# Optimization experiments

Hardware: AMD Instinct MI355X
Metric: run time of the kernel (lower is better)

The kernel has to match this reference:

```python
import jax, jax.numpy as jnp
import numpy as np

NB, H, C, HID, EMB = 4, 12, 1024, 768, 512
E, M, L, SPAN = 22, 4, 16, 32
TD, INTER = 20, 256
NN = E + E * M + L
NREL, NLAYERS = 3, 4

def _build_adj():
    # static relational adjacency: r0 entity<->its mentions, r1 mention<->co-entity mention, r2 mention<->link
    A = np.zeros((NREL, NN, NN), np.float32)
    for e in range(E):
        for m in range(M):
            mi = E + e * M + m
            A[0, e, mi] = A[0, mi, e] = 1.0
            for m2 in range(M):
                if m2 != m:
                    A[1, mi, E + e * M + m2] = 1.0
            li = E + E * M + ((e * M + m) % L)
            A[2, mi, li] = A[2, li, mi] = 1.0
    A = A / (A.sum(-1, keepdims=True) + 1e-5)
    return jnp.asarray(A)

_ADJ = _build_adj()
_TYPES = np.concatenate([np.zeros(E, np.int32), np.ones(E * M, np.int32), np.full(L, 2, np.int32)])

def _forward(sequence_output, attention, W_trans, b_trans, type_embed,
             rgcn_Wrel0, rgcn_Wself0, rgcn_Wrel, rgcn_Wself,
             fs_w1, fs_b1, fs_g1, fs_be1, fs_w2, fs_b2, fs_g2, fs_be2,
             fc_w1, fc_b1, fc_g1, fc_be1, fc_w2, fc_b2, fc_g2, fc_be2,
             cr_w1, cr_b1, cr_w2, cr_b2, cr_w3, cr_b3,
             mention_idx, link_start):
    n = sequence_output.shape[0]
    b = jnp.arange(n)[:, None, None]
    seq = sequence_output @ W_trans + b_trans            # [n,C,EMB] extractor_trans
    attq = attention.transpose(0, 2, 1, 3)               # [n,C,H,C] query-major
    # --- make_graph: mention / entity nodes (gather + logsumexp pooling) ---
    m_rep = seq[b, mention_idx]                          # [n,E,M,EMB]
    m_att = attq[b, mention_idx]                         # [n,E,M,H,C]
    e_rep = jax.nn.logsumexp(m_rep, axis=2)              # [n,E,EMB]
    e_att = m_att.mean(axis=2)                           # [n,E,H,C]
    # --- link nodes: attention-weighted span pooling ---
    idx = link_start[:, :, None] + jnp.arange(SPAN)      # [n,L,SPAN]
    span = seq[b, idx]                                   # [n,L,SPAN,EMB]
    att_rows = attq[b, idx]                              # [n,L,SPAN,H,C]
    col_idx = jnp.broadcast_to(idx[:, :, None, None, :], (n, L, SPAN, H, SPAN))
    block = jnp.take_along_axis(att_rows, col_idx, axis=4).mean(axis=3)  # [n,L,SPAN,SPAN]
    link_rep = jnp.einsum('nlst,nltd->nld', block, span) / SPAN          # [n,L,EMB]
    # --- node matrix + type embedding ---
    nodes = jnp.concatenate([e_rep, m_rep.reshape(n, E * M, EMB), link_rep], axis=1)
    tfeat = jnp.broadcast_to(type_embed[_TYPES][None], (n, NN, TD))
    h = jnp.concatenate([nodes, tfeat], axis=-1)         # [n,NN,EMB+TD]
    # --- RGCN ---
    def rgcn_layer(hh, Wrel, Wself):
        msg = jnp.einsum('rij,njd,rdo->nio', _ADJ, hh, Wrel)
        return jax.nn.relu(msg + hh @ Wself)
    h = rgcn_layer(h, rgcn_Wrel0, rgcn_Wself0)
    for l in range(NLAYERS - 1):
        h = rgcn_layer(h, rgcn_Wrel[l], rgcn_Wself[l])
    # --- relation_map: structure + attention-weighted context ---
    entity_stru = h[:, :E]                               # [n,E,EMB]
    ea = e_att.mean(axis=2)                              # [n,E,C]
    ea = ea / (ea.sum(-1, keepdims=True) + 1e-5)
    e_ctx = jnp.einsum('nec,ncd->ned', ea, seq)          # [n,E,EMB]
    ec = entity_stru + e_ctx
    fmap = (ec[:, :, None, :] * ec[:, None, :, :]).transpose(0, 3, 1, 2)  # [n,EMB,E,E]
    # --- SE fusion (fusion_s / fusion_c, BN in eval form) ---
    conv1x1 = lambda x, w, bb: jnp.einsum('nchw,oc->nohw', x, w) + bb[None, :, None, None]
    bn = lambda x, g, be: x * g[None, :, None, None] + be[None, :, None, None]
    s = bn(conv1x1(jax.nn.relu(bn(conv1x1(fmap, fs_w1, fs_b1), fs_g1, fs_be1)), fs_w2, fs_b2), fs_g2, fs_be2)
    pooled = fmap.mean(axis=(2, 3), keepdims=True)
    cb = bn(conv1x1(jax.nn.relu(bn(conv1x1(pooled, fc_w1, fc_b1), fc_g1, fc_be1)), fc_w2, fc_b2), fc_g2, fc_be2)
    fused = fmap * jax.nn.sigmoid(s + cb)
    # --- conv_reason 5x5 blocks ---
    dn = ('NCHW', 'OIHW', 'NCHW')
    conv = lambda x, w, bb: jax.lax.conv_general_dilated(x, w, (1, 1), 'SAME', dimension_numbers=dn) + bb[None, :, None, None]
    r = jax.nn.relu(conv(fused, cr_w1, cr_b1))
    r = jax.nn.relu(conv(r, cr_w2, cr_b2))
    return jax.nn.relu(conv(r, cr_w3, cr_b3))            # [n,EMB,E,E]

def setup_inputs():
    key = jax.random.key(0)
    ks = jax.random.split(key, 24)
    p = lambda k, sh: jax.random.normal(k, sh, jnp.float32) * 0.02
    z = lambda sh: jnp.zeros(sh, jnp.float32)
    o = lambda sh: jnp.ones(sh, jnp.float32)
    return {
        'sequence_output': jax.random.normal(ks[0], (NB, C, HID), jnp.float32),
        'attention': jax.random.uniform(ks[1], (NB, H, C, C), jnp.float32),
        'W_trans': p(ks[2], (HID, EMB)), 'b_trans': z((EMB,)),
        'type_embed': p(ks[3], (3, TD)),
        'rgcn_Wrel0': p(ks[4], (NREL, EMB + TD, EMB)), 'rgcn_Wself0': p(ks[5], (EMB + TD, EMB)),
        'rgcn_Wrel': p(ks[6], (NLAYERS - 1, NREL, EMB, EMB)), 'rgcn_Wself': p(ks[7], (NLAYERS - 1, EMB, EMB)),
        'fs_w1': p(ks[8], (INTER, EMB)), 'fs_b1': z((INTER,)), 'fs_g1': o((INTER,)), 'fs_be1': z((INTER,)),
        'fs_w2': p(ks[9], (EMB, INTER)), 'fs_b2': z((EMB,)), 'fs_g2': o((EMB,)), 'fs_be2': z((EMB,)),
        'fc_w1': p(ks[10], (INTER, EMB)), 'fc_b1': z((INTER,)), 'fc_g1': o((INTER,)), 'fc_be1': z((INTER,)),
        'fc_w2': p(ks[11], (EMB, INTER)), 'fc_b2': z((EMB,)), 'fc_g2': o((EMB,)), 'fc_be2': z((EMB,)),
        'cr_w1': p(ks[12], (INTER, EMB, 5, 5)), 'cr_b1': z((INTER,)),
        'cr_w2': p(ks[13], (INTER, INTER, 5, 5)), 'cr_b2': z((INTER,)),
        'cr_w3': p(ks[14], (EMB, INTER, 5, 5)), 'cr_b3': z((EMB,)),
        'mention_idx': jax.random.randint(ks[15], (NB, E, M), 0, C),
        'link_start': jnp.sort(jax.random.randint(ks[16], (NB, L), 0, C - SPAN), axis=-1),
    }

def reference(sequence_output, attention, W_trans, b_trans, type_embed,
              rgcn_Wrel0, rgcn_Wself0, rgcn_Wrel, rgcn_Wself,
              fs_w1, fs_b1, fs_g1, fs_be1, fs_w2, fs_b2, fs_g2, fs_be2,
              fc_w1, fc_b1, fc_g1, fc_be1, fc_w2, fc_b2, fc_g2, fc_be2,
              cr_w1, cr_b1, cr_w2, cr_b2, cr_w3, cr_b3,
              mention_idx, link_start):
    return _forward(sequence_output, attention, W_trans, b_trans, type_embed,
                    rgcn_Wrel0, rgcn_Wself0, rgcn_Wrel, rgcn_Wself,
                    fs_w1, fs_b1, fs_g1, fs_be1, fs_w2, fs_b2, fs_g2, fs_be2,
                    fc_w1, fc_b1, fc_g1, fc_be1, fc_w2, fc_b2, fc_g2, fc_be2,
                    cr_w1, cr_b1, cr_w2, cr_b2, cr_w3, cr_b3,
                    mention_idx, link_start)
```

## Files before the change

### kernel.cpp

```cpp
#include <hip/hip_runtime.h>
#include <hip/hip_bf16.h>
#include <stdint.h>

typedef long long ll;
typedef float f32x4 __attribute__((ext_vector_type(4)));
typedef __bf16 bf16x8 __attribute__((ext_vector_type(8)));
typedef __bf16 bf16x4 __attribute__((ext_vector_type(4)));

__global__ void k_prep(const float* __restrict__ cr_w1, const float* __restrict__ cr_w2,
                       const float* __restrict__ cr_w3, __bf16* __restrict__ Wt1,
                       __bf16* __restrict__ Wt2, __bf16* __restrict__ Wt3,
                       const float* __restrict__ W_trans, __bf16* __restrict__ wth,
                       __bf16* __restrict__ wtl,
                       const float* __restrict__ Wrel0, const float* __restrict__ Wself0,
                       __bf16* __restrict__ wc0h, __bf16* __restrict__ wc0l,
                       const float* __restrict__ Wrel, const float* __restrict__ Wself,
                       __bf16* __restrict__ wc13h, __bf16* __restrict__ wc13l)
{
  __shared__ float t[32][33];
  int b = blockIdx.x; int tid = threadIdx.x;
  if (b < 1024){
    const float* w; __bf16* dst; int C, o;
    if (b < 256){ w=cr_w1; dst=Wt1; C=512; o=b; }
    else if (b < 512){ w=cr_w2; dst=Wt2; C=256; o=b-256; }
    else { w=cr_w3; dst=Wt3; C=256; o=b-512; }
    for (int c=tid; c<C; c+=256){
      const float* src = w + ((size_t)o*C + c)*25;
      float v[25];
      #pragma unroll
      for (int q=0;q<25;q++) v[q] = src[q];
      #pragma unroll
      for (int q=0;q<25;q++) dst[((size_t)o*25 + q)*C + c] = (__bf16)v[q];
    }
  } else if (b < 2560){
    ll idx = (ll)(b-1024)*256 + tid;
    int r = (int)(idx % 768); int c = (int)(idx / 768);
    float x = W_trans[(ll)r*512 + c];
    __bf16 h = (__bf16)x;
    wth[idx] = h; wtl[idx] = (__bf16)(x - (float)h);
  } else {
    int Din, Kpad, KD, bx, by;
    const float* wr; const float* ws2; __bf16* hb; __bf16* lb;
    if (b < 3648){
      int b2 = b-2560; bx = b2 % 68; by = b2/68; Din=532; Kpad=2176; KD=544;
      wr = Wrel0; ws2 = Wself0; hb = wc0h; lb = wc0l;
    } else {
      int b3 = b-3648; int l = b3/1024; int r2 = b3%1024; bx = r2%64; by = r2/64;
      Din=512; Kpad=2048; KD=512;
      wr = Wrel + (ll)l*3*512*512; ws2 = Wself + (ll)l*512*512;
      hb = wc13h + (ll)l*512*2048; lb = wc13l + (ll)l*512*2048;
    }
    int k0 = bx*32, o0 = by*32;
    int tx = tid&31, ty = tid>>5;
    for (int j=ty; j<32; j+=8){
      int k = k0 + j; float v = 0.f;
      int r = k / KD, d = k - r*KD;
      if (d < Din && r < 4)
        v = (r<3) ? wr[((ll)(r*Din+d))*512 + o0+tx] : ws2[(ll)d*512 + o0+tx];
      t[j][tx] = v;
    }
    __syncthreads();
    for (int j=ty; j<32; j+=8){
      float x = t[tx][j];
      __bf16 h = (__bf16)x;
      hb[(ll)(o0+j)*Kpad + k0+tx] = h;
      lb[(ll)(o0+j)*Kpad + k0+tx] = (__bf16)(x - (float)h);
    }
  }
}

template<int SPLIT, int MODE, int BN>
__global__ __launch_bounds__(512) void gemm_mfma(
    const float* __restrict__ A,
    const __bf16* __restrict__ Bhi, const __bf16* __restrict__ Blo,
    float* __restrict__ Cf, __bf16* __restrict__ Cb,
    int M, int N, int K, ll sA, ll sB, ll sC,
    const float* __restrict__ biasN, const float* __restrict__ biasM,
    const float* __restrict__ gM, const float* __restrict__ beM,
    const __bf16* __restrict__ Fm, const float* __restrict__ CBV)
{
  constexpr int NF = BN/32;
  constexpr int SL = (4096 + BN*64) * (SPLIT?2:1);
  constexpr int REDB = 256*2*NF*16;
  constexpr int LDSB = (2*SL > REDB) ? 2*SL : REDB;
  __shared__ char lds[LDSB];

  int b = blockIdx.z;
  A += sA*b; Bhi += sB*b; if (SPLIT) Blo += sB*b;

  const int tid = threadIdx.x;
  const int slice = tid>>8;
  const int tl = tid & 255;
  const int w4 = (tid>>6)&3;
  const int grp = tid>>8;
  const int l15 = tid&15, lg=(tid&63)>>4, lg16=lg*16;
  const int wave_m0=(w4>>1)*32, wave_n0=(w4&1)*(BN/2);
  const int m0 = blockIdx.y*64, n0 = blockIdx.x*BN;

  char* sA_H = lds + slice*SL;
  char* sB_H = sA_H + 4096;
  char* sA_L = sB_H + BN*64;
  char* sB_L = sA_L + 4096;

  const int sa_row=tl>>2, sa_c8=tl&3;
  const int sa_byte = sa_row*64 + ((sa_c8*16) ^ (((sa_row>>1)&3)<<4));
  const int gmA = m0 + sa_row;

  int baseA[2], baseB[NF];
  #pragma unroll
  for (int mf=0; mf<2; ++mf){
    int r = wave_m0 + mf*16 + l15;
    baseA[mf] = r*64 + (lg16 ^ (((r>>1)&3)<<4));
  }
  #pragma unroll
  for (int nf=0; nf<NF; ++nf){
    int r = wave_n0 + nf*16 + l15;
    baseB[nf] = r*64 + (lg16 ^ (((r>>1)&3)<<4));
  }

  f32x4 acc[2][NF] = {};

  for (int k0=0; k0<K; k0+=64){
    int kk = k0 + slice*32;
    __syncthreads();
    {
      float f[8] = {0,0,0,0,0,0,0,0};
      if (gmA < M){
        float4 p0 = *reinterpret_cast<const float4*>(A + (ll)gmA*K + kk + sa_c8*8);
        float4 p1 = *reinterpret_cast<const float4*>(A + (ll)gmA*K + kk + sa_c8*8 + 4);
        f[0]=p0.x; f[1]=p0.y; f[2]=p0.z; f[3]=p0.w;
        f[4]=p1.x; f[5]=p1.y; f[6]=p1.z; f[7]=p1.w;
      }
      bf16x8 h, l;
      #pragma unroll
      for (int j=0;j<8;j++){
        h[j] = (__bf16)f[j];
        if (SPLIT) l[j] = (__bf16)(f[j] - (float)h[j]);
      }
      *reinterpret_cast<bf16x8*>(sA_H + sa_byte) = h;
      if (SPLIT) *reinterpret_cast<bf16x8*>(sA_L + sa_byte) = l;
    }
    #pragma unroll
    for (int i=0;i<BN/64;i++){
      int idx = tl + i*256;
      int row = idx>>2, c8 = idx&3;
      int gn = n0 + row;
      int byte = row*64 + ((c8*16) ^ (((row>>1)&3)<<4));
      bf16x8 v = {};
      if (gn < N) v = *reinterpret_cast<const bf16x8*>(Bhi + (ll)gn*K + kk + c8*8);
      *reinterpret_cast<bf16x8*>(sB_H + byte) = v;
      if (SPLIT){
        bf16x8 vl = {};
        if (gn < N) vl = *reinterpret_cast<const bf16x8*>(Blo + (ll)gn*K + kk + c8*8);
        *reinterpret_cast<bf16x8*>(sB_L + byte) = vl;
      }
    }
    __syncthreads();
    bf16x8 aH[2], bH[NF];
    #pragma unroll
    for (int mf=0; mf<2; ++mf) aH[mf] = *reinterpret_cast<const bf16x8*>(sA_H + baseA[mf]);
    #pragma unroll
    for (int nf=0; nf<NF; ++nf) bH[nf] = *reinterpret_cast<const bf16x8*>(sB_H + baseB[nf]);
    if (SPLIT){
      bf16x8 aL[2], bL[NF];
      #pragma unroll
      for (int mf=0; mf<2; ++mf) aL[mf] = *reinterpret_cast<const bf16x8*>(sA_L + baseA[mf]);
      #pragma unroll
      for (int nf=0; nf<NF; ++nf) bL[nf] = *reinterpret_cast<const bf16x8*>(sB_L + baseB[nf]);
      #pragma unroll
      for (int mf=0; mf<2; ++mf)
        #pragma unroll
        for (int nf=0; nf<NF; ++nf){
          acc[mf][nf] = __builtin_amdgcn_mfma_f32_16x16x32_bf16(aH[mf], bH[nf], acc[mf][nf], 0,0,0);
          acc[mf][nf] = __builtin_amdgcn_mfma_f32_16x16x32_bf16(aH[mf], bL[nf], acc[mf][nf], 0,0,0);
          acc[mf][nf] = __builtin_amdgcn_mfma_f32_16x16x32_bf16(aL[mf], bH[nf], acc[mf][nf], 0,0,0);
        }
    } else {
      #pragma unroll
      for (int mf=0; mf<2; ++mf)
        #pragma unroll
        for (int nf=0; nf<NF; ++nf)
          acc[mf][nf] = __builtin_amdgcn_mfma_f32_16x16x32_bf16(aH[mf], bH[nf], acc[mf][nf], 0,0,0);
    }
  }

  __syncthreads();
  if (grp==1){
    char* rp = lds + (ll)(tid-256)*(2*NF*16);
    #pragma unroll
    for (int mf=0; mf<2; ++mf)
      #pragma unroll
      for (int nf=0; nf<NF; ++nf)
        *reinterpret_cast<f32x4*>(rp + (mf*NF+nf)*16) = acc[mf][nf];
  }
  __syncthreads();
  if (grp!=0) return;
  {
    char* rp = lds + (ll)tid*(2*NF*16);
    #pragma unroll
    for (int mf=0; mf<2; ++mf)
      #pragma unroll
      for (int nf=0; nf<NF; ++nf)
        acc[mf][nf] += *reinterpret_cast<f32x4*>(rp + (mf*NF+nf)*16);
  }

  if (MODE==0 || MODE==1){
    float* C = Cf + sC*b;
    #pragma unroll
    for (int mf=0; mf<2; ++mf){
      int gmb = m0 + wave_m0 + mf*16 + lg*4;
      #pragma unroll
      for (int nf=0; nf<NF; ++nf){
        int gn = n0 + wave_n0 + nf*16 + l15;
        if (gn >= N) continue;
        float bn_ = (MODE==0 && biasN) ? biasN[gn] : 0.f;
        f32x4 a = acc[mf][nf];
        #pragma unroll
        for (int r=0;r<4;r++){
          int gm = gmb + r;
          if (gm < M){
            float v = a[r] + bn_;
            if (MODE==1) v = fmaxf(v, 0.f);
            C[(ll)gm*N + gn] = v;
          }
        }
      }
    }
  } else if (MODE==2){
    __bf16* C = Cb + sC*b;
    #pragma unroll
    for (int mf=0; mf<2; ++mf){
      int gmb = m0 + wave_m0 + mf*16 + lg*4;
      float b0=biasM[gmb], b1=biasM[gmb+1], b2=biasM[gmb+2], b3=biasM[gmb+3];
      float g0=gM[gmb], g1=gM[gmb+1], g2=gM[gmb+2], g3=gM[gmb+3];
      float e0=beM[gmb], e1=beM[gmb+1], e2=beM[gmb+2], e3=beM[gmb+3];
      #pragma unroll
      for (int nf=0; nf<NF; ++nf){
        int gn = n0 + wave_n0 + nf*16 + l15;
        if (gn >= N) continue;
        f32x4 a = acc[mf][nf];
        union { bf16x4 v; uint2 u; } pk;
        pk.v[0] = (__bf16)fmaxf((a[0]+b0)*g0+e0, 0.f);
        pk.v[1] = (__bf16)fmaxf((a[1]+b1)*g1+e1, 0.f);
        pk.v[2] = (__bf16)fmaxf((a[2]+b2)*g2+e2, 0.f);
        pk.v[3] = (__bf16)fmaxf((a[3]+b3)*g3+e3, 0.f);
        *reinterpret_cast<uint2*>(C + (ll)gn*M + gmb) = pk.u;
      }
    }
  } else {
    __bf16* C = Cb + sC*b;
    const __bf16* fm = Fm + (ll)b*484*512;
    const float* cb = CBV + (ll)b*512;
    #pragma unroll
    for (int mf=0; mf<2; ++mf){
      int gmb = m0 + wave_m0 + mf*16 + lg*4;
      float b0=biasM[gmb], b1=biasM[gmb+1], b2=biasM[gmb+2], b3=biasM[gmb+3];
      float g0=gM[gmb], g1=gM[gmb+1], g2=gM[gmb+2], g3=gM[gmb+3];
      float e0=beM[gmb], e1=beM[gmb+1], e2=beM[gmb+2], e3=beM[gmb+3];
      float c0=cb[gmb], c1=cb[gmb+1], c2=cb[gmb+2], c3=cb[gmb+3];
      #pragma unroll
      for (int nf=0; nf<NF; ++nf){
        int gn = n0 + wave_n0 + nf*16 + l15;
        if (gn >= N) continue;
        f32x4 a = acc[mf][nf];
        bf16x4 fmv = *reinterpret_cast<const bf16x4*>(fm + (ll)gn*512 + gmb);
        float s0 = (a[0]+b0)*g0+e0 + c0;
        float s1 = (a[1]+b1)*g1+e1 + c1;
        float s2 = (a[2]+b2)*g2+e2 + c2;
        float s3 = (a[3]+b3)*g3+e3 + c3;
        union { bf16x4 v; uint2 u; } pk;
        pk.v[0] = (__bf16)((float)fmv[0] / (1.f + expf(-s0)));
        pk.v[1] = (__bf16)((float)fmv[1] / (1.f + expf(-s1)));
        pk.v[2] = (__bf16)((float)fmv[2] / (1.f + expf(-s2)));
        pk.v[3] = (__bf16)((float)fmv[3] / (1.f + expf(-s3)));
        int py = gn/22, px = gn%22;
        int e = (py+2)*32 + px + 2;
        *reinterpret_cast<uint2*>(C + (ll)e*512 + gmb) = pk.u;
      }
    }
  }
}

template<int CIN, int OCHT, bool FINAL>
__global__ __launch_bounds__(256) void conv5_mfma(
    const __bf16* __restrict__ Xg, const __bf16* __restrict__ Wt,
    const float* __restrict__ bias, __bf16* __restrict__ Xout,
    float* __restrict__ outF)
{
  __shared__ bf16x8 Xs8[272*32/8];
  __shared__ bf16x8 Ws8[5*64*32/8];
  char* xs = (char*)Xs8;
  char* wsm = (char*)Ws8;

  const int tid = threadIdx.x;
  const int l = tid & 63;
  const int l15 = l & 15, lg = l >> 4, lg16 = (l>>4)*16;
  const int w = tid >> 6;
  const int wave_o0 = (w>>1)*32;
  const int wave_p0 = (w&1)*64;
  const int b = blockIdx.z;
  const int p0 = blockIdx.x*128;
  const int o0 = blockIdx.y*64;

  int orow0 = wave_o0 + l15;
  int orow1 = wave_o0 + 16 + l15;
  int baseA0 = orow0*64 + (lg16 ^ (((orow0>>1)&3)<<4));
  int baseA1 = orow1*64 + (lg16 ^ (((orow1>>1)&3)<<4));
  int pl[4];
  #pragma unroll
  for (int pf=0; pf<4; ++pf) pl[pf] = wave_p0 + pf*16 + l15;

  f32x4 acc[2][4] = {};

  const int NCB = CIN/32;
  for (int cblk=0; cblk<NCB; ++cblk){
    __syncthreads();
    #pragma unroll
    for (int i=0;i<5;i++){
      int idx = tid + i*256;
      if (idx < 1088){
        int e = idx>>2, c8 = idx&3;
        const __bf16* g = Xg + ((size_t)(b*928 + p0 + e))*CIN + cblk*32 + c8*8;
        bf16x8 v = *reinterpret_cast<const bf16x8*>(g);
        int byte = e*64 + ((c8*16) ^ (((e>>1)&3)<<4));
        *reinterpret_cast<bf16x8*>(xs + byte) = v;
      }
    }
    for (int g5=0; g5<5; ++g5){
      if (g5>0) __syncthreads();
      #pragma unroll
      for (int i=0;i<5;i++){
        int idx = tid + i*256;
        int tapL = idx>>8, r = idx&255;
        int o = r>>2, c8 = r&3;
        const __bf16* g = Wt + ((size_t)(o0+o)*25 + (g5*5+tapL))*CIN + cblk*32 + c8*8;
        bf16x8 v = *reinterpret_cast<const bf16x8*>(g);
        int byte = tapL*4096 + o*64 + ((c8*16) ^ (((o>>1)&3)<<4));
        *reinterpret_cast<bf16x8*>(wsm + byte) = v;
      }
      __syncthreads();
      #pragma unroll
      for (int tapL=0; tapL<5; ++tapL){
        bf16x8 a0 = *reinterpret_cast<const bf16x8*>(wsm + tapL*4096 + baseA0);
        bf16x8 a1 = *reinterpret_cast<const bf16x8*>(wsm + tapL*4096 + baseA1);
        int koff = g5*32 + tapL;
        #pragma unroll
        for (int pf=0; pf<4; ++pf){
          int e = pl[pf] + koff;
          bf16x8 bv = *reinterpret_cast<const bf16x8*>(xs + e*64 + (lg16 ^ (((e>>1)&3)<<4)));
          acc[0][pf] = __builtin_amdgcn_mfma_f32_16x16x32_bf16(a0, bv, acc[0][pf], 0,0,0);
          acc[1][pf] = __builtin_amdgcn_mfma_f32_16x16x32_bf16(a1, bv, acc[1][pf], 0,0,0);
        }
      }
    }
  }

  #pragma unroll
  for (int of=0; of<2; ++of){
    int og = o0 + wave_o0 + of*16 + lg*4;
    float b0 = bias[og], b1 = bias[og+1], b2 = bias[og+2], b3 = bias[og+3];
    #pragma unroll
    for (int pf=0; pf<4; ++pf){
      int p = p0 + pl[pf];
      int py = p>>5, px = p&31;
      if (py>=22 || px>=22) continue;
      f32x4 a = acc[of][pf];
      float v0 = fmaxf(a[0]+b0, 0.f), v1 = fmaxf(a[1]+b1, 0.f);
      float v2 = fmaxf(a[2]+b2, 0.f), v3 = fmaxf(a[3]+b3, 0.f);
      if (FINAL){
        size_t base = ((size_t)b*OCHT + og)*484 + py*22 + px;
        outF[base] = v0; outF[base+484] = v1; outF[base+968] = v2; outF[base+1452] = v3;
      } else {
        union { bf16x4 v; uint2 u; } pk;
        pk.v[0] = (__bf16)v0; pk.v[1] = (__bf16)v1; pk.v[2] = (__bf16)v2; pk.v[3] = (__bf16)v3;
        int e = p + 66;
        *reinterpret_cast<uint2*>(Xout + ((size_t)(b*928 + e))*OCHT + og) = pk.u;
      }
    }
  }
}

__global__ void k_gather(const float* __restrict__ seq, const float* __restrict__ att,
                         const int* __restrict__ midx, const int* __restrict__ ls_,
                         const float* __restrict__ te, float* __restrict__ h0,
                         float* __restrict__ ectx)
{
  __shared__ float part[32][8];
  __shared__ float wv[32];
  __shared__ float vals[1024];
  __shared__ float red[256];
  int b = blockIdx.x; int t = threadIdx.x;
  if (b < 88){
    int n = b/22, e = b%22;
    int rows[4];
    #pragma unroll
    for (int m=0;m<4;m++) rows[m] = midx[(n*22+e)*4+m];
    for (int d=t; d<512; d+=256){
      float v[4]; float mx = -1e30f;
      #pragma unroll
      for (int m=0;m<4;m++){
        v[m] = seq[((ll)n*1024+rows[m])*512 + d];
        h0[((ll)n*126+22+e*4+m)*532 + d] = v[m];
        mx = fmaxf(mx, v[m]);
      }
      float s = 0.f;
      #pragma unroll
      for (int m=0;m<4;m++) s += expf(v[m]-mx);
      h0[((ll)n*126+e)*532 + d] = mx + logf(s);
    }
  } else if (b < 152){
    int bb = b-88;
    int n = bb/16, l = bb%16;
    int ls = ls_[n*16+l];
    int tt = t>>3, lane = t&7;
    float acc = 0.f;
    for (int i=lane; i<384; i+=8){
      int h = i>>5, s = i&31;
      acc += att[((ll)(n*12+h)*1024 + ls+s)*1024 + (ls+tt)];
    }
    part[tt][lane] = acc; __syncthreads();
    if (lane==0){
      float s2=0.f;
      #pragma unroll
      for (int q=0;q<8;q++) s2 += part[tt][q];
      wv[tt] = s2*(1.f/12.f);
    }
    __syncthreads();
    for (int d=t; d<512; d+=256){
      float a2 = 0.f;
      for (int tk=0;tk<32;tk++) a2 += wv[tk]*seq[((ll)n*1024+ls+tk)*512 + d];
      h0[((ll)n*126+110+l)*532 + d] = a2*(1.f/32.f);
    }
  } else if (b < 192){
    int idx = (b-152)*256 + t;
    if (idx < 4*126*20){
      int q = idx%20; int i = (idx/20)%126; int n = idx/(20*126);
      int ty = (i<22)?0:((i<110)?1:2);
      h0[((ll)n*126+i)*532 + 512 + q] = te[ty*20+q];
    }
  } else {
    int bb = b-192;
    int n = bb/22, e = bb%22;
    int rows[4];
    #pragma unroll
    for (int m=0;m<4;m++) rows[m] = midx[(n*22+e)*4+m];
    float local = 0.f;
    for (int c=t; c<1024; c+=256){
      float acc = 0.f;
      #pragma unroll
      for (int m=0;m<4;m++){
        const float* base = att + ((ll)n*12*1024 + rows[m])*1024 + c;
        #pragma unroll
        for (int h=0;h<12;h++) acc += base[(ll)h*1048576];
      }
      acc *= (1.f/48.f);
      vals[c] = acc; local += acc;
    }
    red[t] = local; __syncthreads();
    for (int s=128;s>0;s>>=1){ if (t<s) red[t]+=red[t+s]; __syncthreads(); }
    float inv = 1.f/(red[0] + 1e-5f);
    for (int c=t; c<1024; c+=256) vals[c] *= inv;
    __syncthreads();
    float a0 = 0.f, a1 = 0.f;
    #pragma unroll 4
    for (int c=0;c<1024;c++){
      float v = vals[c];
      const float* s = seq + ((ll)n*1024+c)*512;
      a0 += v*s[t]; a1 += v*s[t+256];
    }
    ectx[((ll)n*22+e)*512 + t]       = a0;
    ectx[((ll)n*22+e)*512 + t + 256] = a1;
  }
}

__global__ void k_buildX_s(const float* __restrict__ h, float* __restrict__ X,
                           int Din, int KD){
  int n = blockIdx.x/126, i = blockIdx.x%126;
  const float* hb = h + (ll)n*126*Din;
  ll rowoff = (ll)(n*126+i)*4*KD;
  const float inv1 = 1.f/(1.f+1e-5f), inv3 = 1.f/(3.f+1e-5f), inv4 = 1.f/(4.f+1e-5f);
  for (int d=threadIdx.x; d<KD; d+=256){
    float m0v=0.f, m1v=0.f, m2v=0.f, hh=0.f;
    if (d < Din){
      if (i < 22){
        int base = 22 + i*4;
        float s = hb[(ll)(base+0)*Din+d] + hb[(ll)(base+1)*Din+d]
                + hb[(ll)(base+2)*Din+d] + hb[(ll)(base+3)*Din+d];
        m0v = s * inv4;
      } else if (i < 110){
        int em = i-22, e = em>>2, base = 22+(e<<2);
        m0v = hb[(ll)e*Din+d] * inv1;
        float s1 = 0.f;
        #pragma unroll
        for (int m2=0;m2<4;m2++) if (base+m2 != i) s1 += hb[(ll)(base+m2)*Din+d];
        m1v = s1 * inv3;
        m2v = hb[(ll)(110+(em&15))*Din+d] * inv1;
      } else {
        int li0 = i-110;
        int cnt = (li0<8)?6:5;
        float s = 0.f;
        for (int t2=0;t2<cnt;t2++) s += hb[(ll)(22+li0+16*t2)*Din+d];
        m2v = s / ((float)cnt + 1e-5f);
      }
      hh = hb[(ll)i*Din+d];
    }
    X[rowoff + 0*KD + d] = m0v;
    X[rowoff + 1*KD + d] = m1v;
    X[rowoff + 2*KD + d] = m2v;
    X[rowoff + 3*KD + d] = hh;
  }
}

__global__ void k_fmap2(const float* __restrict__ hfin, const float* __restrict__ ectx,
                        __bf16* __restrict__ fmapT,
                        const float* __restrict__ w1, const float* __restrict__ b1,
                        const float* __restrict__ g1, const float* __restrict__ be1,
                        const float* __restrict__ w2, const float* __restrict__ b2,
                        const float* __restrict__ g2, const float* __restrict__ be2,
                        float* __restrict__ cb){
  __shared__ float ps[512], t1[256];
  int b = blockIdx.x; int t = threadIdx.x;
  if (b < 3872){
    int idx = b*256 + t;
    int ch = idx & 511; int p = (idx>>9) % 484; int n = idx/(484*512);
    int i = p/22, j = p%22;
    float vi = hfin[((ll)n*126+i)*512 + ch] + ectx[((ll)n*22+i)*512 + ch];
    float vj = hfin[((ll)n*126+j)*512 + ch] + ectx[((ll)n*22+j)*512 + ch];
    fmapT[idx] = (__bf16)(vi*vj);
  } else {
    int n = b-3872;
    for (int c=t; c<512; c+=256){
      float s = 0.f;
      for (int i=0;i<22;i++)
        s += hfin[((ll)n*126+i)*512 + c] + ectx[((ll)n*22+i)*512 + c];
      ps[c] = s*s*(1.f/484.f);
    }
    __syncthreads();
    {
      float acc = 0.f;
      for (int c=0;c<512;c++) acc += w1[t*512+c]*ps[c];
      float v = g1[t]*(acc+b1[t]) + be1[t];
      t1[t] = fmaxf(v, 0.f);
    }
    __syncthreads();
    for (int o=t; o<512; o+=256){
      float acc = 0.f;
      for (int c=0;c<256;c++) acc += w2[o*256+c]*t1[c];
      cb[n*512+o] = g2[o]*(acc+b2[o]) + be2[o];
    }
  }
}

extern "C" void kernel_launch(void* const* d_in, const int* in_sizes, int n_in,
                              void* d_out, int out_size, void* d_ws, size_t ws_size,
                              hipStream_t stream)
{
  (void)in_sizes; (void)n_in; (void)out_size; (void)ws_size;
  const float* seqout   = (const float*)d_in[0];
  const float* att      = (const float*)d_in[1];
  const float* W_trans  = (const float*)d_in[2];
  const float* b_trans  = (const float*)d_in[3];
  const float* type_emb = (const float*)d_in[4];
  const float* Wrel0    = (const float*)d_in[5];
  const float* Wself0   = (const float*)d_in[6];
  const float* Wrel     = (const float*)d_in[7];
  const float* Wself    = (const float*)d_in[8];
  const float* fs_w1    = (const float*)d_in[9];
  const float* fs_b1    = (const float*)d_in[10];
  const float* fs_g1    = (const float*)d_in[11];
  const float* fs_be1   = (const float*)d_in[12];
  const float* fs_w2    = (const float*)d_in[13];
  const float* fs_b2    = (const float*)d_in[14];
  const float* fs_g2    = (const float*)d_in[15];
  const float* fs_be2   = (const float*)d_in[16];
  const float* fc_w1    = (const float*)d_in[17];
  const float* fc_b1    = (const float*)d_in[18];
  const float* fc_g1    = (const float*)d_in[19];
  const float* fc_be1   = (const float*)d_in[20];
  const float* fc_w2    = (const float*)d_in[21];
  const float* fc_b2    = (const float*)d_in[22];
  const float* fc_g2    = (const float*)d_in[23];
  const float* fc_be2   = (const float*)d_in[24];
  const float* cr_w1    = (const float*)d_in[25];
  const float* cr_b1    = (const float*)d_in[26];
  const float* cr_w2    = (const float*)d_in[27];
  const float* cr_b2    = (const float*)d_in[28];
  const float* cr_w3    = (const float*)d_in[29];
  const float* cr_b3    = (const float*)d_in[30];
  const int*   midx     = (const int*)d_in[31];
  const int*   lstart   = (const int*)d_in[32];
  float* out            = (float*)d_out;

  char* wsb = (char*)d_ws;
  size_t off = 0;
  auto allocB = [&](size_t nbytes)->char*{ char* p = wsb + off; off += (nbytes + 63) & ~(size_t)63; return p; };
  float* seq   = (float*)allocB((size_t)4096*512*4);
  float* h0    = (float*)allocB((size_t)504*532*4);
  float* ectx  = (float*)allocB((size_t)88*512*4);
  float* X     = (float*)allocB((size_t)504*2176*4);
  float* hA    = (float*)allocB((size_t)504*512*4);
  float* hB    = (float*)allocB((size_t)504*512*4);
  float* cbv   = (float*)allocB(2048*4);
  __bf16* wth  = (__bf16*)allocB((size_t)512*768*2);
  __bf16* wtl  = (__bf16*)allocB((size_t)512*768*2);
  __bf16* wc0h = (__bf16*)allocB((size_t)512*2176*2);
  __bf16* wc0l = (__bf16*)allocB((size_t)512*2176*2);
  __bf16* wc13h= (__bf16*)allocB((size_t)3*512*2048*2);
  __bf16* wc13l= (__bf16*)allocB((size_t)3*512*2048*2);
  __bf16* fmapT= (__bf16*)allocB((size_t)4*484*512*2);
  __bf16* s1bT = (__bf16*)allocB((size_t)4*484*256*2);
  __bf16* Xint1 = (__bf16*)allocB((size_t)4*928*512*2);
  __bf16* Xint2 = (__bf16*)allocB((size_t)4*928*256*2);
  __bf16* Xint3 = (__bf16*)allocB((size_t)4*928*256*2);
  __bf16* Wt1   = (__bf16*)allocB((size_t)256*25*512*2);
  __bf16* Wt2   = (__bf16*)allocB((size_t)256*25*256*2);
  __bf16* Wt3   = (__bf16*)allocB((size_t)512*25*256*2);

  (void)hipMemsetAsync(Xint1, 0, (size_t)(4*928*512 + 4*928*256 + 4*928*256)*2, stream);

  k_prep<<<6720,256,0,stream>>>(cr_w1, cr_w2, cr_w3, Wt1, Wt2, Wt3,
                                W_trans, wth, wtl,
                                Wrel0, Wself0, wc0h, wc0l,
                                Wrel, Wself, wc13h, wc13l);

  gemm_mfma<1,0,128><<<dim3(4,64,1),512,0,stream>>>(seqout, wth, wtl, seq, nullptr,
      4096,512,768, 0,0,0, b_trans,nullptr,nullptr,nullptr, nullptr,nullptr);
  k_gather<<<280,256,0,stream>>>(seq, att, midx, lstart, type_emb, h0, ectx);
  k_buildX_s<<<504,256,0,stream>>>(h0, X, 532, 544);
  gemm_mfma<1,1,64><<<dim3(8,8,1),512,0,stream>>>(X, wc0h, wc0l, hA, nullptr,
      504,512,2176, 0,0,0, nullptr,nullptr,nullptr,nullptr, nullptr,nullptr);
  float* hcur = hA; float* hnxt = hB;
  for (int l=0;l<3;l++){
    k_buildX_s<<<504,256,0,stream>>>(hcur, X, 512, 512);
    gemm_mfma<1,1,64><<<dim3(8,8,1),512,0,stream>>>(X,
        wc13h + (ll)l*512*2048, wc13l + (ll)l*512*2048, hnxt, nullptr,
        504,512,2048, 0,0,0, nullptr,nullptr,nullptr,nullptr, nullptr,nullptr);
    float* t = hcur; hcur = hnxt; hnxt = t;
  }
  k_fmap2<<<3876,256,0,stream>>>(hcur, ectx, fmapT,
                                 fc_w1, fc_b1, fc_g1, fc_be1,
                                 fc_w2, fc_b2, fc_g2, fc_be2, cbv);
  gemm_mfma<0,2,64><<<dim3(8,4,4),512,0,stream>>>(fs_w1, fmapT, nullptr, nullptr, s1bT,
      256,484,512, 0, (ll)484*512, (ll)484*256,
      nullptr, fs_b1, fs_g1, fs_be1, nullptr,nullptr);
  gemm_mfma<0,4,64><<<dim3(8,8,4),512,0,stream>>>(fs_w2, s1bT, nullptr, nullptr, Xint1,
      512,484,256, 0, (ll)484*256, (ll)928*512,
      nullptr, fs_b2, fs_g2, fs_be2, fmapT, cbv);
  conv5_mfma<512,256,false><<<dim3(6,4,4),256,0,stream>>>(Xint1, Wt1, cr_b1, Xint2, nullptr);
  conv5_mfma<256,256,false><<<dim3(6,4,4),256,0,stream>>>(Xint2, Wt2, cr_b2, Xint3, nullptr);
  conv5_mfma<256,512,true ><<<dim3(6,8,4),256,0,stream>>>(Xint3, Wt3, cr_b3, nullptr, out);
}
```

Measured before the change: 567.9 us.

## Compute entity context via MFMA GEMM and fuse pairwise feature map into GEMMs

```diff
diff --git a/kernel.cpp b/kernel.cpp
--- a/kernel.cpp
+++ b/kernel.cpp
@@ -69,7 +69,7 @@
   }
 }
 
-template<int SPLIT, int MODE, int BN>
+template<int SPLIT, int MODE, int BN, int FMAPB>
 __global__ __launch_bounds__(512) void gemm_mfma(
     const float* __restrict__ A,
     const __bf16* __restrict__ Bhi, const __bf16* __restrict__ Blo,
@@ -77,7 +77,8 @@
     int M, int N, int K, ll sA, ll sB, ll sC,
     const float* __restrict__ biasN, const float* __restrict__ biasM,
     const float* __restrict__ gM, const float* __restrict__ beM,
-    const __bf16* __restrict__ Fm, const float* __restrict__ CBV)
+    const float* __restrict__ Hf, const float* __restrict__ Ec,
+    const float* __restrict__ CBV)
 {
   constexpr int NF = BN/32;
   constexpr int SL = (4096 + BN*64) * (SPLIT?2:1);
@@ -86,7 +87,8 @@
   __shared__ char lds[LDSB];
 
   int b = blockIdx.z;
-  A += sA*b; Bhi += sB*b; if (SPLIT) Blo += sB*b;
+  A += sA*b;
+  if (!FMAPB){ Bhi += sB*b; if (SPLIT) Blo += sB*b; }
 
   const int tid = threadIdx.x;
   const int slice = tid>>8;
@@ -146,13 +148,39 @@
       int row = idx>>2, c8 = idx&3;
       int gn = n0 + row;
       int byte = row*64 + ((c8*16) ^ (((row>>1)&3)<<4));
-      bf16x8 v = {};
-      if (gn < N) v = *reinterpret_cast<const bf16x8*>(Bhi + (ll)gn*K + kk + c8*8);
-      *reinterpret_cast<bf16x8*>(sB_H + byte) = v;
-      if (SPLIT){
-        bf16x8 vl = {};
-        if (gn < N) vl = *reinterpret_cast<const bf16x8*>(Blo + (ll)gn*K + kk + c8*8);
-        *reinterpret_cast<bf16x8*>(sB_L + byte) = vl;
+      if (FMAPB){
+        bf16x8 v = {};
+        if (gn < N){
+          int pi = gn/22, pj = gn%22;
+          const float* hi_ = Hf + ((ll)b*126+pi)*512 + kk + c8*8;
+          const float* ei_ = Ec + ((ll)b*22 +pi)*512 + kk + c8*8;
+          const float* hj_ = Hf + ((ll)b*126+pj)*512 + kk + c8*8;
+          const float* ej_ = Ec + ((ll)b*22 +pj)*512 + kk + c8*8;
+          float4 ha = *reinterpret_cast<const float4*>(hi_);
+          float4 hb2 = *reinterpret_cast<const float4*>(hi_+4);
+          float4 ea = *reinterpret_cast<const float4*>(ei_);
+          float4 eb = *reinterpret_cast<const float4*>(ei_+4);
+          float4 hc = *reinterpret_cast<const float4*>(hj_);
+          float4 hd = *reinterpret_cast<const float4*>(hj_+4);
+          float4 ec2 = *reinterpret_cast<const float4*>(ej_);
+          float4 ed = *reinterpret_cast<const float4*>(ej_+4);
+          float vi[8] = {ha.x+ea.x, ha.y+ea.y, ha.z+ea.z, ha.w+ea.w,
+                         hb2.x+eb.x, hb2.y+eb.y, hb2.z+eb.z, hb2.w+eb.w};
+          float vj[8] = {hc.x+ec2.x, hc.y+ec2.y, hc.z+ec2.z, hc.w+ec2.w,
+                         hd.x+ed.x, hd.y+ed.y, hd.z+ed.z, hd.w+ed.w};
+          #pragma unroll
+          for (int q=0;q<8;q++) v[q] = (__bf16)(vi[q]*vj[q]);
+        }
+        *reinterpret_cast<bf16x8*>(sB_H + byte) = v;
+      } else {
+        bf16x8 v = {};
+        if (gn < N) v = *reinterpret_cast<const bf16x8*>(Bhi + (ll)gn*K + kk + c8*8);
+        *reinterpret_cast<bf16x8*>(sB_H + byte) = v;
+        if (SPLIT){
+          bf16x8 vl = {};
+          if (gn < N) vl = *reinterpret_cast<const bf16x8*>(Blo + (ll)gn*K + kk + c8*8);
+          *reinterpret_cast<bf16x8*>(sB_L + byte) = vl;
+        }
       }
     }
     __syncthreads();
@@ -249,7 +277,6 @@
     }
   } else {
     __bf16* C = Cb + sC*b;
-    const __bf16* fm = Fm + (ll)b*484*512;
     const float* cb = CBV + (ll)b*512;
     #pragma unroll
     for (int mf=0; mf<2; ++mf){
@@ -263,16 +290,24 @@
         int gn = n0 + wave_n0 + nf*16 + l15;
         if (gn >= N) continue;
         f32x4 a = acc[mf][nf];
-        bf16x4 fmv = *reinterpret_cast<const bf16x4*>(fm + (ll)gn*512 + gmb);
+        int pi = gn/22, pj = gn%22;
+        float4 hi4 = *reinterpret_cast<const float4*>(Hf + ((ll)b*126+pi)*512 + gmb);
+        float4 ei4 = *reinterpret_cast<const float4*>(Ec + ((ll)b*22 +pi)*512 + gmb);
+        float4 hj4 = *reinterpret_cast<const float4*>(Hf + ((ll)b*126+pj)*512 + gmb);
+        float4 ej4 = *reinterpret_cast<const float4*>(Ec + ((ll)b*22 +pj)*512 + gmb);
+        float fm0 = (hi4.x+ei4.x)*(hj4.x+ej4.x);
+        float fm1 = (hi4.y+ei4.y)*(hj4.y+ej4.y);
+        float fm2 = (hi4.z+ei4.z)*(hj4.z+ej4.z);
+        float fm3 = (hi4.w+ei4.w)*(hj4.w+ej4.w);
         float s0 = (a[0]+b0)*g0+e0 + c0;
         float s1 = (a[1]+b1)*g1+e1 + c1;
         float s2 = (a[2]+b2)*g2+e2 + c2;
         float s3 = (a[3]+b3)*g3+e3 + c3;
         union { bf16x4 v; uint2 u; } pk;
-        pk.v[0] = (__bf16)((float)fmv[0] / (1.f + expf(-s0)));
-        pk.v[1] = (__bf16)((float)fmv[1] / (1.f + expf(-s1)));
-        pk.v[2] = (__bf16)((float)fmv[2] / (1.f + expf(-s2)));
-        pk.v[3] = (__bf16)((float)fmv[3] / (1.f + expf(-s3)));
+        pk.v[0] = (__bf16)(fm0 / (1.f + expf(-s0)));
+        pk.v[1] = (__bf16)(fm1 / (1.f + expf(-s1)));
+        pk.v[2] = (__bf16)(fm2 / (1.f + expf(-s2)));
+        pk.v[3] = (__bf16)(fm3 / (1.f + expf(-s3)));
         int py = gn/22, px = gn%22;
         int e = (py+2)*32 + px + 2;
         *reinterpret_cast<uint2*>(C + (ll)e*512 + gmb) = pk.u;
@@ -383,12 +418,14 @@
 __global__ void k_gather(const float* __restrict__ seq, const float* __restrict__ att,
                          const int* __restrict__ midx, const int* __restrict__ ls_,
                          const float* __restrict__ te, float* __restrict__ h0,
-                         float* __restrict__ ectx)
+                         float* __restrict__ ea, __bf16* __restrict__ sqTh,
+                         __bf16* __restrict__ sqTl)
 {
   __shared__ float part[32][8];
   __shared__ float wv[32];
   __shared__ float vals[1024];
   __shared__ float red[256];
+  __shared__ float tt2[32][33];
   int b = blockIdx.x; int t = threadIdx.x;
   if (b < 88){
     int n = b/22, e = b%22;
@@ -438,7 +475,7 @@
       int ty = (i<22)?0:((i<110)?1:2);
       h0[((ll)n*126+i)*532 + 512 + q] = te[ty*20+q];
     }
-  } else {
+  } else if (b < 280){
     int bb = b-192;
     int n = bb/22, e = bb%22;
     int rows[4];
@@ -458,18 +495,22 @@
     }
     red[t] = local; __syncthreads();
     for (int s=128;s>0;s>>=1){ if (t<s) red[t]+=red[t+s]; __syncthreads(); }
-    float inv = 1.f/(red[0] + 1e-5f);
-    for (int c=t; c<1024; c+=256) vals[c] *= inv;
+    float denom = red[0] + 1e-5f;
+    for (int c=t; c<1024; c+=256) ea[((ll)bb)*1024 + c] = vals[c]/denom;
+  } else {
+    int b2 = b-280;
+    int n = b2>>9; int rem = b2&511;
+    int r0 = (rem&31)*32, c0 = (rem>>5)*32;
+    int tx = t&31, ty = t>>5;
+    for (int j=ty; j<32; j+=8)
+      tt2[j][tx] = seq[((ll)n*1024 + r0+j)*512 + c0+tx];
     __syncthreads();
-    float a0 = 0.f, a1 = 0.f;
-    #pragma unroll 4
-    for (int c=0;c<1024;c++){
-      float v = vals[c];
-      const float* s = seq + ((ll)n*1024+c)*512;
-      a0 += v*s[t]; a1 += v*s[t+256];
-    }
-    ectx[((ll)n*22+e)*512 + t]       = a0;
-    ectx[((ll)n*22+e)*512 + t + 256] = a1;
+    for (int j=ty; j<32; j+=8){
+      float x = tt2[tx][j];
+      __bf16 h = (__bf16)x;
+      ll o = ((ll)n*512 + c0+j)*1024 + r0+tx;
+      sqTh[o] = h; sqTl[o] = (__bf16)(x - (float)h);
+    }
   }
 }
 
@@ -511,43 +552,32 @@
   }
 }
 
-__global__ void k_fmap2(const float* __restrict__ hfin, const float* __restrict__ ectx,
-                        __bf16* __restrict__ fmapT,
-                        const float* __restrict__ w1, const float* __restrict__ b1,
-                        const float* __restrict__ g1, const float* __restrict__ be1,
-                        const float* __restrict__ w2, const float* __restrict__ b2,
-                        const float* __restrict__ g2, const float* __restrict__ be2,
-                        float* __restrict__ cb){
+__global__ void k_poolcb(const float* __restrict__ hfin, const float* __restrict__ ectx,
+                         const float* __restrict__ w1, const float* __restrict__ b1,
+                         const float* __restrict__ g1, const float* __restrict__ be1,
+                         const float* __restrict__ w2, const float* __restrict__ b2,
+                         const float* __restrict__ g2, const float* __restrict__ be2,
+                         float* __restrict__ cb){
   __shared__ float ps[512], t1[256];
-  int b = blockIdx.x; int t = threadIdx.x;
-  if (b < 3872){
-    int idx = b*256 + t;
-    int ch = idx & 511; int p = (idx>>9) % 484; int n = idx/(484*512);
-    int i = p/22, j = p%22;
-    float vi = hfin[((ll)n*126+i)*512 + ch] + ectx[((ll)n*22+i)*512 + ch];
-    float vj = hfin[((ll)n*126+j)*512 + ch] + ectx[((ll)n*22+j)*512 + ch];
-    fmapT[idx] = (__bf16)(vi*vj);
-  } else {
-    int n = b-3872;
-    for (int c=t; c<512; c+=256){
-      float s = 0.f;
-      for (int i=0;i<22;i++)
-        s += hfin[((ll)n*126+i)*512 + c] + ectx[((ll)n*22+i)*512 + c];
-      ps[c] = s*s*(1.f/484.f);
-    }
-    __syncthreads();
-    {
-      float acc = 0.f;
-      for (int c=0;c<512;c++) acc += w1[t*512+c]*ps[c];
-      float v = g1[t]*(acc+b1[t]) + be1[t];
-      t1[t] = fmaxf(v, 0.f);
-    }
-    __syncthreads();
-    for (int o=t; o<512; o+=256){
-      float acc = 0.f;
-      for (int c=0;c<256;c++) acc += w2[o*256+c]*t1[c];
-      cb[n*512+o] = g2[o]*(acc+b2[o]) + be2[o];
-    }
+  int n = blockIdx.x; int t = threadIdx.x;
+  for (int c=t; c<512; c+=256){
+    float s = 0.f;
+    for (int i=0;i<22;i++)
+      s += hfin[((ll)n*126+i)*512 + c] + ectx[((ll)n*22+i)*512 + c];
+    ps[c] = s*s*(1.f/484.f);
+  }
+  __syncthreads();
+  {
+    float acc = 0.f;
+    for (int c=0;c<512;c++) acc += w1[t*512+c]*ps[c];
+    float v = g1[t]*(acc+b1[t]) + be1[t];
+    t1[t] = fmaxf(v, 0.f);
+  }
+  __syncthreads();
+  for (int o=t; o<512; o+=256){
+    float acc = 0.f;
+    for (int c=0;c<256;c++) acc += w2[o*256+c]*t1[c];
+    cb[n*512+o] = g2[o]*(acc+b2[o]) + be2[o];
   }
 }
 
@@ -596,6 +626,7 @@
   auto allocB = [&](size_t nbytes)->char*{ char* p = wsb + off; off += (nbytes + 63) & ~(size_t)63; return p; };
   float* seq   = (float*)allocB((size_t)4096*512*4);
   float* h0    = (float*)allocB((size_t)504*532*4);
+  float* ea    = (float*)allocB((size_t)88*1024*4);
   float* ectx  = (float*)allocB((size_t)88*512*4);
   float* X     = (float*)allocB((size_t)504*2176*4);
   float* hA    = (float*)allocB((size_t)504*512*4);
@@ -603,11 +634,12 @@
   float* cbv   = (float*)allocB(2048*4);
   __bf16* wth  = (__bf16*)allocB((size_t)512*768*2);
   __bf16* wtl  = (__bf16*)allocB((size_t)512*768*2);
+  __bf16* sqTh = (__bf16*)allocB((size_t)4*512*1024*2);
+  __bf16* sqTl = (__bf16*)allocB((size_t)4*512*1024*2);
   __bf16* wc0h = (__bf16*)allocB((size_t)512*2176*2);
   __bf16* wc0l = (__bf16*)allocB((size_t)512*2176*2);
   __bf16* wc13h= (__bf16*)allocB((size_t)3*512*2048*2);
   __bf16* wc13l= (__bf16*)allocB((size_t)3*512*2048*2);
-  __bf16* fmapT= (__bf16*)allocB((size_t)4*484*512*2);
   __bf16* s1bT = (__bf16*)allocB((size_t)4*484*256*2);
   __bf16* Xint1 = (__bf16*)allocB((size_t)4*928*512*2);
   __bf16* Xint2 = (__bf16*)allocB((size_t)4*928*256*2);
@@ -623,29 +655,31 @@
                                 Wrel0, Wself0, wc0h, wc0l,
                                 Wrel, Wself, wc13h, wc13l);
 
-  gemm_mfma<1,0,128><<<dim3(4,64,1),512,0,stream>>>(seqout, wth, wtl, seq, nullptr,
-      4096,512,768, 0,0,0, b_trans,nullptr,nullptr,nullptr, nullptr,nullptr);
-  k_gather<<<280,256,0,stream>>>(seq, att, midx, lstart, type_emb, h0, ectx);
+  gemm_mfma<1,0,128,0><<<dim3(4,64,1),512,0,stream>>>(seqout, wth, wtl, seq, nullptr,
+      4096,512,768, 0,0,0, b_trans,nullptr,nullptr,nullptr, nullptr,nullptr,nullptr);
+  k_gather<<<2328,256,0,stream>>>(seq, att, midx, lstart, type_emb, h0, ea, sqTh, sqTl);
+  gemm_mfma<1,0,64,0><<<dim3(8,1,4),512,0,stream>>>(ea, sqTh, sqTl, ectx, nullptr,
+      22,512,1024, (ll)22*1024, (ll)512*1024, (ll)22*512,
+      nullptr,nullptr,nullptr,nullptr, nullptr,nullptr,nullptr);
   k_buildX_s<<<504,256,0,stream>>>(h0, X, 532, 544);
-  gemm_mfma<1,1,64><<<dim3(8,8,1),512,0,stream>>>(X, wc0h, wc0l, hA, nullptr,
-      504,512,2176, 0,0,0, nullptr,nullptr,nullptr,nullptr, nullptr,nullptr);
+  gemm_mfma<1,1,64,0><<<dim3(8,8,1),512,0,stream>>>(X, wc0h, wc0l, hA, nullptr,
+      504,512,2176, 0,0,0, nullptr,nullptr,nullptr,nullptr, nullptr,nullptr,nullptr);
   float* hcur = hA; float* hnxt = hB;
   for (int l=0;l<3;l++){
     k_buildX_s<<<504,256,0,stream>>>(hcur, X, 512, 512);
-    gemm_mfma<1,1,64><<<dim3(8,8,1),512,0,stream>>>(X,
+    gemm_mfma<1,1,64,0><<<dim3(8,8,1),512,0,stream>>>(X,
         wc13h + (ll)l*512*2048, wc13l + (ll)l*512*2048, hnxt, nullptr,
-        504,512,2048, 0,0,0, nullptr,nullptr,nullptr,nullptr, nullptr,nullptr);
+        504,512,2048, 0,0,0, nullptr,nullptr,nullptr,nullptr, nullptr,nullptr,nullptr);
     float* t = hcur; hcur = hnxt; hnxt = t;
   }
-  k_fmap2<<<3876,256,0,stream>>>(hcur, ectx, fmapT,
-                                 fc_w1, fc_b1, fc_g1, fc_be1,
-                                 fc_w2, fc_b2, fc_g2, fc_be2, cbv);
-  gemm_mfma<0,2,64><<<dim3(8,4,4),512,0,stream>>>(fs_w1, fmapT, nullptr, nullptr, s1bT,
-      256,484,512, 0, (ll)484*512, (ll)484*256,
-      nullptr, fs_b1, fs_g1, fs_be1, nullptr,nullptr);
-  gemm_mfma<0,4,64><<<dim3(8,8,4),512,0,stream>>>(fs_w2, s1bT, nullptr, nullptr, Xint1,
+  k_poolcb<<<4,256,0,stream>>>(hcur, ectx, fc_w1, fc_b1, fc_g1, fc_be1,
+                               fc_w2, fc_b2, fc_g2, fc_be2, cbv);
+  gemm_mfma<0,2,64,1><<<dim3(8,4,4),512,0,stream>>>(fs_w1, nullptr, nullptr, nullptr, s1bT,
+      256,484,512, 0, 0, (ll)484*256,
+      nullptr, fs_b1, fs_g1, fs_be1, hcur, ectx, nullptr);
+  gemm_mfma<0,4,64,0><<<dim3(8,8,4),512,0,stream>>>(fs_w2, s1bT, nullptr, nullptr, Xint1,
       512,484,256, 0, (ll)484*256, (ll)928*512,
-      nullptr, fs_b2, fs_g2, fs_be2, fmapT, cbv);
+      nullptr, fs_b2, fs_g2, fs_be2, hcur, ectx, cbv);
   conv5_mfma<512,256,false><<<dim3(6,4,4),256,0,stream>>>(Xint1, Wt1, cr_b1, Xint2, nullptr);
   conv5_mfma<256,256,false><<<dim3(6,4,4),256,0,stream>>>(Xint2, Wt2, cr_b2, Xint3, nullptr);
   conv5_mfma<256,512,true ><<<dim3(6,8,4),256,0,stream>>>(Xint3, Wt3, cr_b3, nullptr, out);
```

Result: faster. 535.9 us (-5.6%).
